# Performance work log

Hardware: AMD Instinct MI355X
Metric: run time of the kernel (lower is better)

Reference implementation:

```python
import jax, jax.numpy as jnp
import numpy as np

N_NODES = 20000
N_EDGES = 160000
N_GRAPHS = 64
IN_DIM = 1304  # 1280 + 24
NEG_SLOPE = 0.2


def gat_conv(x, src, dst, W, a_src, a_dst, b, heads, out_ch):
    """PyG-style GATConv (source_to_target flow, self loops already appended).
    x: [N, in], W: [in, heads*out], a_src/a_dst: [heads, out], b: [heads*out].
    Returns [N, heads*out] (concat=True)."""
    N = x.shape[0]
    h = (x @ W).reshape(N, heads, out_ch)                 # [N, H, C]
    e_src = jnp.sum(h * a_src[None], axis=-1)             # [N, H]
    e_dst = jnp.sum(h * a_dst[None], axis=-1)             # [N, H]
    e = jax.nn.leaky_relu(e_src[src] + e_dst[dst], NEG_SLOPE)  # [E, H]
    # softmax over incoming edges of each destination node
    e_max = jax.ops.segment_max(e, dst, num_segments=N)   # [N, H]
    e_exp = jnp.exp(e - e_max[dst])
    denom = jax.ops.segment_sum(e_exp, dst, num_segments=N)
    alpha = e_exp / (denom[dst] + 1e-16)                  # [E, H]
    msg = h[src] * alpha[:, :, None]                      # [E, H, C]
    out = jax.ops.segment_sum(msg, dst, num_segments=N)   # [N, H, C]
    return out.reshape(N, heads * out_ch) + b


def setup_inputs() -> dict:
    key = jax.random.key(0)
    ks = jax.random.split(key, 20)
    x = jax.random.normal(ks[0], (N_NODES, IN_DIM), dtype=jnp.float32)
    edge_index = jax.random.randint(ks[1], (2, N_EDGES), 0, N_NODES, dtype=jnp.int32)
    phy = jax.random.normal(ks[2], (N_GRAPHS, 188), dtype=jnp.float32)
    batch = jnp.sort(jax.random.randint(ks[3], (N_NODES,), 0, N_GRAPHS, dtype=jnp.int32))

    def glorot(k, shape):
        fan_in, fan_out = shape[0], shape[-1]
        lim = jnp.sqrt(6.0 / (fan_in + fan_out))
        return jax.random.uniform(k, shape, jnp.float32, -lim, lim)

    params = {
        # conv1: GATConv(1304, 256, heads=3)
        "W1": glorot(ks[4], (IN_DIM, 3 * 256)),
        "a_src1": glorot(ks[5], (3, 256)) * 0.1,
        "a_dst1": glorot(ks[6], (3, 256)) * 0.1,
        "b1": jnp.zeros((3 * 256,), jnp.float32),
        # conv2: GATConv(768, 256, heads=1)
        "W2": glorot(ks[7], (3 * 256, 256)),
        "a_src2": glorot(ks[8], (1, 256)) * 0.1,
        "a_dst2": glorot(ks[9], (1, 256)) * 0.1,
        "b2": jnp.zeros((256,), jnp.float32),
        # fc1
        "fc1_w1": glorot(ks[10], (188, 128)), "fc1_b1": jnp.zeros((128,), jnp.float32),
        "fc1_w2": glorot(ks[11], (128, 128)), "fc1_b2": jnp.zeros((128,), jnp.float32),
        # fc2
        "fc2_w1": glorot(ks[12], (256 + 128, 192)), "fc2_b1": jnp.zeros((192,), jnp.float32),
        "fc2_w2": glorot(ks[13], (192, 2)), "fc2_b2": jnp.zeros((2,), jnp.float32),
    }
    return {"x": x, "edge_index": edge_index, "phy": phy, "batch": batch, **params}


def reference(x, edge_index, phy, batch,
              W1, a_src1, a_dst1, b1,
              W2, a_src2, a_dst2, b2,
              fc1_w1, fc1_b1, fc1_w2, fc1_b2,
              fc2_w1, fc2_b1, fc2_w2, fc2_b2):
    N = x.shape[0]
    # add self loops (PyG GATConv default)
    loops = jnp.arange(N, dtype=edge_index.dtype)
    src = jnp.concatenate([edge_index[0], loops])
    dst = jnp.concatenate([edge_index[1], loops])

    h = gat_conv(x, src, dst, W1, a_src1, a_dst1, b1, heads=3, out_ch=256)
    h = jax.nn.relu(h)  # dropout is identity at inference
    h = gat_conv(h, src, dst, W2, a_src2, a_dst2, b2, heads=1, out_ch=256)

    # global mean pool per graph
    sums = jax.ops.segment_sum(h, batch, num_segments=N_GRAPHS)        # [B, 256]
    cnts = jax.ops.segment_sum(jnp.ones((N,), h.dtype), batch, num_segments=N_GRAPHS)
    pooled = sums / jnp.maximum(cnts, 1.0)[:, None]

    mid = jax.nn.relu(phy @ fc1_w1 + fc1_b1)
    mid = jax.nn.relu(mid @ fc1_w2 + fc1_b2)

    z = jnp.concatenate([pooled, mid], axis=1)                          # [B, 384]
    z = jax.nn.relu(z @ fc2_w1 + fc2_b1)
    logits = z @ fc2_w2 + fc2_b2
    return jax.nn.softmax(logits, axis=1)
```

## Files before the change

### kernel.cpp

```cpp
#include <hip/hip_runtime.h>
#include <hip/hip_bf16.h>
#include <math.h>

#define NN    20000
#define MP1   20224
#define NP    20096
#define E0    160000
#define EL    180000
#define NG    64
#define INDIM 1304
#define K1P   1344
#define GNT   21
#define GNX   3
#define GMB   79
#define NEG_SLOPE 0.2f
#define PCH   8

typedef __bf16 bf16x8 __attribute__((ext_vector_type(8)));
typedef __bf16 bf16x4 __attribute__((ext_vector_type(4)));
typedef float  f32x4  __attribute__((ext_vector_type(4)));

__device__ __forceinline__ void gload16(const void* g, void* l) {
    __builtin_amdgcn_global_load_lds(
        (const __attribute__((address_space(1))) void*)g,
        (__attribute__((address_space(3))) void*)l, 16, 0, 0);
}

#define BAR()  { __builtin_amdgcn_s_barrier(); asm volatile("" ::: "memory"); }
#define VMW(n) { asm volatile("s_waitcnt vmcnt(" #n ")" ::: "memory"); __builtin_amdgcn_sched_barrier(0); }

__device__ __forceinline__ void stA(const __hip_bfloat16* __restrict__ A, int bm, int kt, int mh,
                                    char* abuf, int w, int l) {
#pragma unroll
    for (int u = 0; u < 2; u++) {
        int rl = (w << 3) + (l >> 3);
        int lrow = u * 128 + mh * 64 + rl;
        int skb = ((l & 7) << 4) ^ ((rl & 7) << 4);
        const char* g = (const char*)(A + (size_t)(bm + lrow) * K1P + kt * 64) + skb;
        gload16(g, abuf + (u * 128 + mh * 64) * 128 + (w << 10));
    }
}

__device__ __forceinline__ void stB(const __hip_bfloat16* __restrict__ Bt, int bn, int kt, int nh,
                                    char* bbuf, int w, int l) {
#pragma unroll
    for (int u = 0; u < 2; u++) {
        int c = u * 2 + (w >> 2);
        int row0 = c * 64 + nh * 32;
        int rl = ((w & 3) << 3) + (l >> 3);
        int skb = ((l & 7) << 4) ^ ((rl & 7) << 4);
        const char* g = (const char*)(Bt + (size_t)(bn + row0 + rl) * K1P + kt * 64) + skb;
        gload16(g, bbuf + row0 * 128 + ((w & 3) << 10));
    }
}

__global__ __launch_bounds__(512)
void gemm256(const __hip_bfloat16* __restrict__ A,
             const __hip_bfloat16* __restrict__ Bt,
             __hip_bfloat16* __restrict__ C, int M) {
    __shared__ char lds[131072];
    const int t = threadIdx.x;
    const int w = t >> 6, l = t & 63;
    const int wm = w >> 2, wn = w & 3;
    const int fr = l & 15, fq = l >> 4;
    const int amask = (fr & 7) << 4;

    const int nwg = GMB * GNX;
    const int q8 = nwg >> 3, r8 = nwg & 7;
    const int xcd = blockIdx.x & 7, sub = blockIdx.x >> 3;
    const int logical = (xcd < r8 ? xcd * (q8 + 1) : r8 * (q8 + 1) + (xcd - r8) * q8) + sub;
    const int bm = (logical / GNX) * 256;
    const int bn = (logical % GNX) * 256;

    f32x4 acc[8][4];
#pragma unroll
    for (int i = 0; i < 8; i++)
#pragma unroll
        for (int j = 0; j < 4; j++) acc[i][j] = (f32x4){0.f, 0.f, 0.f, 0.f};

    char* A0 = lds;            char* B0 = lds + 32768;
    char* A1 = lds + 65536;    char* B1 = lds + 98304;

    stA(A, bm, 0, 0, A0, w, l);
    stB(Bt, bn, 0, 0, B0, w, l);
    stA(A, bm, 0, 1, A0, w, l);
    stB(Bt, bn, 0, 1, B0, w, l);
    stA(A, bm, 1, 0, A1, w, l);
    stB(Bt, bn, 1, 0, B1, w, l);
    VMW(8);
    BAR();

    for (int kt = 0; kt < GNT; kt++) {
        char* Ab = lds + (kt & 1) * 65536;
        char* Bb = Ab + 32768;
        char* An = lds + ((kt + 1) & 1) * 65536;
        char* Bn = An + 32768;
        bf16x8 a_c[4][2], b_c0[2][2], b_c1[2][2];

#pragma unroll
        for (int im = 0; im < 4; im++)
#pragma unroll
            for (int kk = 0; kk < 2; kk++)
                a_c[im][kk] = *(const bf16x8*)(Ab + (wm * 128 + im * 16 + fr) * 128 + ((kk * 64 + fq * 16) ^ amask));
#pragma unroll
        for (int jn = 0; jn < 2; jn++)
#pragma unroll
            for (int kk = 0; kk < 2; kk++)
                b_c0[jn][kk] = *(const bf16x8*)(Bb + (wn * 64 + jn * 16 + fr) * 128 + ((kk * 64 + fq * 16) ^ amask));
        if (kt + 1 < GNT) stA(A, bm, kt + 1, 1, An, w, l);
        BAR();
        __builtin_amdgcn_s_setprio(1);
#pragma unroll
        for (int im = 0; im < 4; im++)
#pragma unroll
            for (int jn = 0; jn < 2; jn++)
#pragma unroll
                for (int kk = 0; kk < 2; kk++)
                    acc[im][jn] = __builtin_amdgcn_mfma_f32_16x16x32_bf16(a_c[im][kk], b_c0[jn][kk], acc[im][jn], 0, 0, 0);
        __builtin_amdgcn_s_setprio(0);
        if (kt == GNT - 1) { VMW(0); } else { VMW(6); }
        BAR();

#pragma unroll
        for (int jn = 0; jn < 2; jn++)
#pragma unroll
            for (int kk = 0; kk < 2; kk++)
                b_c1[jn][kk] = *(const bf16x8*)(Bb + (wn * 64 + 32 + jn * 16 + fr) * 128 + ((kk * 64 + fq * 16) ^ amask));
        if (kt + 1 < GNT) stB(Bt, bn, kt + 1, 1, Bn, w, l);
        BAR();
        __builtin_amdgcn_s_setprio(1);
#pragma unroll
        for (int im = 0; im < 4; im++)
#pragma unroll
            for (int jn = 0; jn < 2; jn++)
#pragma unroll
                for (int kk = 0; kk < 2; kk++)
                    acc[im][2 + jn] = __builtin_amdgcn_mfma_f32_16x16x32_bf16(a_c[im][kk], b_c1[jn][kk], acc[im][2 + jn], 0, 0, 0);
        __builtin_amdgcn_s_setprio(0);
        if (kt == GNT - 1) { VMW(2); } else { VMW(10); }
        BAR();

#pragma unroll
        for (int im = 0; im < 4; im++)
#pragma unroll
            for (int kk = 0; kk < 2; kk++)
                a_c[im][kk] = *(const bf16x8*)(Ab + (wm * 128 + 64 + im * 16 + fr) * 128 + ((kk * 64 + fq * 16) ^ amask));
        if (kt + 2 < GNT) stA(A, bm, kt + 2, 0, Ab, w, l);
        BAR();
        __builtin_amdgcn_s_setprio(1);
#pragma unroll
        for (int im = 0; im < 4; im++)
#pragma unroll
            for (int jn = 0; jn < 2; jn++)
#pragma unroll
                for (int kk = 0; kk < 2; kk++)
                    acc[4 + im][jn] = __builtin_amdgcn_mfma_f32_16x16x32_bf16(a_c[im][kk], b_c0[jn][kk], acc[4 + im][jn], 0, 0, 0);
        __builtin_amdgcn_s_setprio(0);
        BAR();

        if (kt + 2 < GNT) stB(Bt, bn, kt + 2, 0, Bb, w, l);
        BAR();
        __builtin_amdgcn_s_setprio(1);
#pragma unroll
        for (int im = 0; im < 4; im++)
#pragma unroll
            for (int jn = 0; jn < 2; jn++)
#pragma unroll
                for (int kk = 0; kk < 2; kk++)
                    acc[4 + im][2 + jn] = __builtin_amdgcn_mfma_f32_16x16x32_bf16(a_c[im][kk], b_c1[jn][kk], acc[4 + im][2 + jn], 0, 0, 0);
        __builtin_amdgcn_s_setprio(0);
        if (kt + 2 < GNT) { VMW(8); }
        else if (kt + 2 == GNT) { VMW(4); }
        BAR();
    }

#pragma unroll
    for (int i = 0; i < 8; i++)
#pragma unroll
        for (int j = 0; j < 4; j++)
#pragma unroll
            for (int r = 0; r < 4; r++) {
                int row = bm + wm * 128 + i * 16 + fq * 4 + r;
                int col = bn + wn * 64 + j * 16 + fr;
                if (row < M) C[(size_t)row * 768 + col] = __float2bfloat16(acc[i][j][r]);
            }
}

template<typename CT>
__global__ __launch_bounds__(256)
void mfma_gemm(const __hip_bfloat16* __restrict__ A,
               const __hip_bfloat16* __restrict__ Bt,
               CT* __restrict__ C,
               int M, int N, int K, int NX) {
    __shared__ __hip_bfloat16 As[128 * 32];
    __shared__ __hip_bfloat16 Bs[128 * 32];
    const int t = threadIdx.x;
    const int w = t >> 6;
    const int l = t & 63;

    const int nwg = gridDim.x;
    const int q = nwg >> 3, r = nwg & 7;
    const int xcd = blockIdx.x & 7, idx = blockIdx.x >> 3;
    const int logical = (xcd < r ? xcd * (q + 1) : r * (q + 1) + (xcd - r) * q) + idx;
    const int bm = (logical / NX) * 128;
    const int bn = (logical % NX) * 128;

    const int wm = (w >> 1) * 64;
    const int wn = (w & 1) * 64;

    f32x4 acc[4][4];
#pragma unroll
    for (int i = 0; i < 4; i++)
#pragma unroll
        for (int j = 0; j < 4; j++) acc[i][j] = (f32x4){0.f, 0.f, 0.f, 0.f};

    const int sr = t >> 2;
    const int sc = (t & 3) * 8;
    const __hip_bfloat16* a0 = A  + (size_t)(bm + sr)      * K + sc;
    const __hip_bfloat16* a1 = A  + (size_t)(bm + 64 + sr) * K + sc;
    const __hip_bfloat16* b0 = Bt + (size_t)(bn + sr)      * K + sc;
    const __hip_bfloat16* b1 = Bt + (size_t)(bn + 64 + sr) * K + sc;
    char* asw0 = (char*)As + w * 1024;
    char* asw1 = (char*)As + 4096 + w * 1024;
    char* bsw0 = (char*)Bs + w * 1024;
    char* bsw1 = (char*)Bs + 4096 + w * 1024;

    const int fr = l & 15;
    const int fq = l >> 4;

    for (int k0 = 0; k0 < K; k0 += 32) {
        gload16(a0 + k0, asw0);
        gload16(a1 + k0, asw1);
        gload16(b0 + k0, bsw0);
        gload16(b1 + k0, bsw1);
        __syncthreads();
        bf16x8 av[4], bv[4];
#pragma unroll
        for (int i = 0; i < 4; i++)
            av[i] = *(const bf16x8*)&As[(wm + i * 16 + fr) * 32 + fq * 8];
#pragma unroll
        for (int j = 0; j < 4; j++)
            bv[j] = *(const bf16x8*)&Bs[(wn + j * 16 + fr) * 32 + fq * 8];
#pragma unroll
        for (int i = 0; i < 4; i++)
#pragma unroll
            for (int j = 0; j < 4; j++)
                acc[i][j] = __builtin_amdgcn_mfma_f32_16x16x32_bf16(av[i], bv[j], acc[i][j], 0, 0, 0);
        __syncthreads();
    }

#pragma unroll
    for (int i = 0; i < 4; i++) {
#pragma unroll
        for (int j = 0; j < 4; j++) {
#pragma unroll
            for (int r2 = 0; r2 < 4; r2++) {
                int row = bm + wm + i * 16 + fq * 4 + r2;
                int col = bn + wn + j * 16 + fr;
                if (row < M) {
                    if constexpr (sizeof(CT) == 2)
                        C[(size_t)row * N + col] = __float2bfloat16(acc[i][j][r2]);
                    else
                        C[(size_t)row * N + col] = acc[i][j][r2];
                }
            }
        }
    }
}

__global__ __launch_bounds__(256)
void convert_x(const float* __restrict__ X, __hip_bfloat16* __restrict__ Xb) {
    int idx = blockIdx.x * 256 + threadIdx.x;
    const int nb = K1P / 8;
    if (idx >= MP1 * nb) return;
    int row = idx / nb;
    int cb = (idx - row * nb) * 8;
    union { __hip_bfloat16 h[8]; float4 f4; } u;
    if (row < NN && cb + 8 <= INDIM) {
        const float4* p = (const float4*)(X + (size_t)row * INDIM + cb);
        float4 u0 = p[0], u1 = p[1];
        u.h[0] = __float2bfloat16(u0.x); u.h[1] = __float2bfloat16(u0.y);
        u.h[2] = __float2bfloat16(u0.z); u.h[3] = __float2bfloat16(u0.w);
        u.h[4] = __float2bfloat16(u1.x); u.h[5] = __float2bfloat16(u1.y);
        u.h[6] = __float2bfloat16(u1.z); u.h[7] = __float2bfloat16(u1.w);
    } else {
#pragma unroll
        for (int e = 0; e < 8; e++) {
            float f = (row < NN && cb + e < INDIM) ? X[(size_t)row * INDIM + cb + e] : 0.f;
            u.h[e] = __float2bfloat16(f);
        }
    }
    *(float4*)(Xb + (size_t)row * K1P + cb) = u.f4;
}

__global__ __launch_bounds__(256)
void convert_wT(const float* __restrict__ W, __hip_bfloat16* __restrict__ Wt,
                int K, int N, int Kp) {
    int idx = blockIdx.x * 256 + threadIdx.x;
    if (idx >= N * Kp) return;
    int n = idx / Kp, k = idx - n * Kp;
    float f = (k < K) ? W[(size_t)k * N + n] : 0.f;
    Wt[idx] = __float2bfloat16(f);
}

template<int H>
__global__ __launch_bounds__(256)
void compute_e(const __hip_bfloat16* __restrict__ hfeat, const float* __restrict__ a_src,
               const float* __restrict__ a_dst, float* __restrict__ esrc,
               float* __restrict__ edst, int N) {
    const int wv = threadIdx.x >> 6, lane = threadIdx.x & 63;
    const int n = blockIdx.x * 4 + wv;
    if (n >= N) return;
#pragma unroll
    for (int hd = 0; hd < H; hd++) {
        bf16x4 hv = *(const bf16x4*)(hfeat + (size_t)n * (H * 256) + hd * 256 + lane * 4);
        float ps = 0.f, pd = 0.f;
#pragma unroll
        for (int e = 0; e < 4; e++) {
            float f = (float)hv[e];
            ps += f * a_src[hd * 256 + lane * 4 + e];
            pd += f * a_dst[hd * 256 + lane * 4 + e];
        }
#pragma unroll
        for (int o = 32; o > 0; o >>= 1) {
            ps += __shfl_down(ps, o, 64);
            pd += __shfl_down(pd, o, 64);
        }
        if (lane == 0) {
            esrc[n * H + hd] = ps;
            edst[n * H + hd] = pd;
        }
    }
}

__global__ void hist_kernel(const int* __restrict__ ei, int* __restrict__ deg) {
    int e = blockIdx.x * 256 + threadIdx.x;
    if (e >= EL) return;
    int d = (e < E0) ? ei[E0 + e] : (e - E0);
    atomicAdd(&deg[d], 1);
}

__global__ __launch_bounds__(1024)
void scan_kernel(const int* __restrict__ deg, int* __restrict__ off) {
    __shared__ int wsum[16];
    __shared__ int carry_s;
    int t = threadIdx.x, lane = t & 63, wv = t >> 6;
    if (t == 0) { carry_s = 0; off[0] = 0; }
    __syncthreads();
    for (int base = 0; base < NN; base += 1024) {
        int i = base + t;
        int v = (i < NN) ? deg[i] : 0;
        int x = v;
#pragma unroll
        for (int o = 1; o < 64; o <<= 1) {
            int y = __shfl_up(x, o, 64);
            if (lane >= o) x += y;
        }
        if (lane == 63) wsum[wv] = x;
        __syncthreads();
        if (wv == 0 && lane < 16) {
            int s = wsum[lane];
#pragma unroll
            for (int o = 1; o < 16; o <<= 1) {
                int y = __shfl_up(s, o, 64);
                if (lane >= o) s += y;
            }
            wsum[lane] = s;
        }
        __syncthreads();
        int woff = (wv == 0) ? 0 : wsum[wv - 1];
        int total = wsum[15];
        if (i < NN) off[i + 1] = carry_s + woff + x;
        __syncthreads();
        if (t == 0) carry_s += total;
        __syncthreads();
    }
}

__global__ void fill_kernel(const int* __restrict__ ei, const int* __restrict__ off,
                            int* __restrict__ cur, int* __restrict__ csr) {
    int e = blockIdx.x * 256 + threadIdx.x;
    if (e >= EL) return;
    int d = (e < E0) ? ei[E0 + e] : (e - E0);
    int s = (e < E0) ? ei[e] : (e - E0);
    int pos = off[d] + atomicAdd(&cur[d], 1);
    csr[pos] = s;
}

template<int H, bool RELU, typename OutT>
__global__ __launch_bounds__(256)
void gat_aggregate(const __hip_bfloat16* __restrict__ hfeat,
                   const float* __restrict__ esrc,
                   const float* __restrict__ edst,
                   const int* __restrict__ off, const int* __restrict__ csr,
                   const float* __restrict__ bias,
                   OutT* __restrict__ out, int N) {
    const int wv = threadIdx.x >> 6, lane = threadIdx.x & 63;
    const int n = blockIdx.x * 4 + wv;
    if (n >= N) return;
    const int beg = off[n];
    const int deg = off[n + 1] - beg;

    float ed[H], m[H], den[H];
    f32x4 acc[H];
#pragma unroll
    for (int h = 0; h < H; h++) {
        ed[h] = edst[n * H + h];
        m[h] = -INFINITY;
        den[h] = 0.f;
        acc[h] = (f32x4){0.f, 0.f, 0.f, 0.f};
    }

    for (int base = 0; base < deg; base += 64) {
        const int i = base + lane;
        int s = 0;
        float lg[H];
        if (i < deg) {
            s = csr[beg + i];
#pragma unroll
            for (int h = 0; h < H; h++) {
                float v = esrc[s * H + h] + ed[h];
                lg[h] = (v >= 0.f) ? v : NEG_SLOPE * v;
            }
        } else {
#pragma unroll
            for (int h = 0; h < H; h++) lg[h] = -INFINITY;
        }
        float cm[H];
#pragma unroll
        for (int h = 0; h < H; h++) {
            cm[h] = lg[h];
#pragma unroll
            for (int o = 1; o < 64; o <<= 1)
                cm[h] = fmaxf(cm[h], __shfl_xor(cm[h], o, 64));
        }
#pragma unroll
        for (int h = 0; h < H; h++) {
            float nm = fmaxf(m[h], cm[h]);
            float sc = expf(m[h] - nm);
            den[h] *= sc;
#pragma unroll
            for (int e = 0; e < 4; e++) acc[h][e] *= sc;
            m[h] = nm;
        }
        float wgt[H];
#pragma unroll
        for (int h = 0; h < H; h++) {
            wgt[h] = (i < deg) ? expf(lg[h] - m[h]) : 0.f;
            den[h] += wgt[h];
        }
        const int cnt = min(64, deg - base);
        for (int j = 0; j < cnt; j++) {
            int sj = __shfl(s, j, 64);
#pragma unroll
            for (int h = 0; h < H; h++) {
                float wj = __shfl(wgt[h], j, 64);
                bf16x4 hv = *(const bf16x4*)(hfeat + (size_t)sj * (H * 256) + h * 256 + 4 * lane);
#pragma unroll
                for (int e = 0; e < 4; e++) acc[h][e] += wj * (float)hv[e];
            }
        }
    }
#pragma unroll
    for (int h = 0; h < H; h++) {
#pragma unroll
        for (int o = 1; o < 64; o <<= 1) den[h] += __shfl_xor(den[h], o, 64);
    }
#pragma unroll
    for (int h = 0; h < H; h++) {
        float inv = 1.f / (den[h] + 1e-16f);
        if constexpr (sizeof(OutT) == 2) {
            bf16x4 r;
#pragma unroll
            for (int e = 0; e < 4; e++) {
                float f = acc[h][e] * inv + bias[h * 256 + 4 * lane + e];
                if (RELU) f = fmaxf(f, 0.f);
                r[e] = (__bf16)f;
            }
            *(bf16x4*)((__hip_bfloat16*)out + (size_t)n * (H * 256) + h * 256 + 4 * lane) = r;
        } else {
            float4 r;
            float* rp = &r.x;
#pragma unroll
            for (int e = 0; e < 4; e++) {
                float f = acc[h][e] * inv + bias[h * 256 + 4 * lane + e];
                if (RELU) f = fmaxf(f, 0.f);
                rp[e] = f;
            }
            *(float4*)((float*)out + (size_t)n * (H * 256) + h * 256 + 4 * lane) = r;
        }
    }
}

__device__ __forceinline__ int lower_bound_batch(const int* __restrict__ batch, int key) {
    int lo = 0, hi = NN;
    while (lo < hi) {
        int mid = (lo + hi) >> 1;
        if (batch[mid] < key) lo = mid + 1; else hi = mid;
    }
    return lo;
}

__global__ __launch_bounds__(256)
void pool_partial(const float* __restrict__ out2, const int* __restrict__ batch,
                  float* __restrict__ partial, float* __restrict__ cnts) {
    const int g = blockIdx.x, c = blockIdx.y, t = threadIdx.x;
    const int s = lower_bound_batch(batch, g);
    const int e = lower_bound_batch(batch, g + 1);
    float acc = 0.f;
    for (int n = s + c; n < e; n += PCH) acc += out2[(size_t)n * 256 + t];
    partial[((size_t)g * PCH + c) * 256 + t] = acc;
    if (t == 0 && c == 0) cnts[g] = (float)(e - s);
}

__global__ __launch_bounds__(256)
void head_kernel(const float* __restrict__ phy, const float* __restrict__ partial,
                 const float* __restrict__ cnts,
                 const float* __restrict__ w11, const float* __restrict__ b11,
                 const float* __restrict__ w12, const float* __restrict__ b12,
                 const float* __restrict__ w21, const float* __restrict__ b21,
                 const float* __restrict__ w22, const float* __restrict__ b22,
                 float* __restrict__ out) {
    int g = blockIdx.x, t = threadIdx.x;
    __shared__ float ph[188];
    __shared__ float z[384];
    __shared__ float mid[128];
    __shared__ float t1[192];
    __shared__ float lg[2];
    if (t < 188) ph[t] = phy[g * 188 + t];
    {
        float s = 0.f;
#pragma unroll
        for (int c = 0; c < PCH; c++) s += partial[((size_t)g * PCH + c) * 256 + t];
        z[t] = s / fmaxf(cnts[g], 1.0f);
    }
    __syncthreads();
    if (t < 128) {
        float s = b11[t];
        for (int k = 0; k < 188; k++) s += ph[k] * w11[k * 128 + t];
        mid[t] = fmaxf(s, 0.f);
    }
    __syncthreads();
    if (t < 128) {
        float s = b12[t];
        for (int k = 0; k < 128; k++) s += mid[k] * w12[k * 128 + t];
        z[256 + t] = fmaxf(s, 0.f);
    }
    __syncthreads();
    if (t < 192) {
        float s = b21[t];
        for (int k = 0; k < 384; k++) s += z[k] * w21[k * 192 + t];
        t1[t] = fmaxf(s, 0.f);
    }
    __syncthreads();
    if (t < 2) {
        float s = b22[t];
        for (int k = 0; k < 192; k++) s += t1[k] * w22[k * 2 + t];
        lg[t] = s;
    }
    __syncthreads();
    if (t == 0) {
        float mx = fmaxf(lg[0], lg[1]);
        float e0 = expf(lg[0] - mx), e1 = expf(lg[1] - mx);
        float d = e0 + e1;
        out[g * 2 + 0] = e0 / d;
        out[g * 2 + 1] = e1 / d;
    }
}

extern "C" void kernel_launch(void* const* d_in, const int* in_sizes, int n_in,
                              void* d_out, int out_size, void* d_ws, size_t ws_size,
                              hipStream_t stream) {
    const float* x       = (const float*)d_in[0];
    const int*   ei      = (const int*)  d_in[1];
    const float* phy     = (const float*)d_in[2];
    const int*   batch   = (const int*)  d_in[3];
    const float* W1      = (const float*)d_in[4];
    const float* a_src1  = (const float*)d_in[5];
    const float* a_dst1  = (const float*)d_in[6];
    const float* b1      = (const float*)d_in[7];
    const float* W2      = (const float*)d_in[8];
    const float* a_src2  = (const float*)d_in[9];
    const float* a_dst2  = (const float*)d_in[10];
    const float* b2      = (const float*)d_in[11];
    const float* fc1_w1  = (const float*)d_in[12];
    const float* fc1_b1  = (const float*)d_in[13];
    const float* fc1_w2  = (const float*)d_in[14];
    const float* fc1_b2  = (const float*)d_in[15];
    const float* fc2_w1  = (const float*)d_in[16];
    const float* fc2_b1  = (const float*)d_in[17];
    const float* fc2_w2  = (const float*)d_in[18];
    const float* fc2_b2  = (const float*)d_in[19];
    float* out = (float*)d_out;

    char* base = (char*)d_ws;
    size_t o = 0;
    auto alloc = [&](size_t bytes) { size_t r = o; o += (bytes + 255) & ~255ULL; return r; };

    size_t o_xb   = alloc((size_t)MP1 * K1P * 2);
    size_t o_w1t  = alloc((size_t)768 * K1P * 2);
    size_t o_w2t  = alloc((size_t)256 * 768 * 2);
    size_t o_h1b  = alloc((size_t)NP * 768 * 2);
    size_t o_hob  = alloc((size_t)NP * 768 * 2);
    size_t o_es1  = alloc((size_t)NN * 3 * 4);
    size_t o_ed1  = alloc((size_t)NN * 3 * 4);
    size_t o_es2  = alloc((size_t)NN * 4);
    size_t o_ed2  = alloc((size_t)NN * 4);
    size_t o_deg  = alloc((size_t)(NN + 1) * 4);
    size_t o_off  = alloc((size_t)(NN + 1) * 4);
    size_t o_cur  = alloc((size_t)NN * 4);
    size_t o_csr  = alloc((size_t)EL * 4);
    size_t o_part = alloc((size_t)NG * PCH * 256 * 4);
    size_t o_cnts = alloc((size_t)NG * 4);

    __hip_bfloat16* xb   = (__hip_bfloat16*)(base + o_xb);
    __hip_bfloat16* w1t  = (__hip_bfloat16*)(base + o_w1t);
    __hip_bfloat16* w2t  = (__hip_bfloat16*)(base + o_w2t);
    __hip_bfloat16* h1b  = (__hip_bfloat16*)(base + o_h1b);
    __hip_bfloat16* hob  = (__hip_bfloat16*)(base + o_hob);
    __hip_bfloat16* h2b  = (__hip_bfloat16*)(base + o_xb);
    float*          out2 = (float*)(base + o_xb + (size_t)24 * 1024 * 1024);
    float* es1   = (float*)(base + o_es1);
    float* ed1   = (float*)(base + o_ed1);
    float* es2   = (float*)(base + o_es2);
    float* ed2   = (float*)(base + o_ed2);
    int*   deg   = (int*)(base + o_deg);
    int*   offs  = (int*)(base + o_off);
    int*   cur   = (int*)(base + o_cur);
    int*   csr   = (int*)(base + o_csr);
    float* part  = (float*)(base + o_part);
    float* cnts  = (float*)(base + o_cnts);

    hipMemsetAsync(deg, 0, (size_t)(NN + 1) * 4, stream);
    hipMemsetAsync(cur, 0, (size_t)NN * 4, stream);
    hipMemsetAsync(hob + (size_t)NN * 768, 0, (size_t)(NP - NN) * 768 * 2, stream);

    convert_x<<<(MP1 * (K1P / 8) + 255) / 256, 256, 0, stream>>>(x, xb);
    convert_wT<<<(768 * K1P + 255) / 256, 256, 0, stream>>>(W1, w1t, INDIM, 768, K1P);
    convert_wT<<<(256 * 768 + 255) / 256, 256, 0, stream>>>(W2, w2t, 768, 256, 768);

    hist_kernel<<<(EL + 255) / 256, 256, 0, stream>>>(ei, deg);
    scan_kernel<<<1, 1024, 0, stream>>>(deg, offs);
    fill_kernel<<<(EL + 255) / 256, 256, 0, stream>>>(ei, offs, cur, csr);

    gemm256<<<GMB * GNX, 512, 0, stream>>>(xb, w1t, h1b, NN);
    compute_e<3><<<(NN + 3) / 4, 256, 0, stream>>>(h1b, a_src1, a_dst1, es1, ed1, NN);
    gat_aggregate<3, true, __hip_bfloat16><<<(NN + 3) / 4, 256, 0, stream>>>(h1b, es1, ed1, offs, csr, b1, hob, NN);

    mfma_gemm<__hip_bfloat16><<<2 * 157, 256, 0, stream>>>(hob, w2t, h2b, NN, 256, 768, 2);
    compute_e<1><<<(NN + 3) / 4, 256, 0, stream>>>(h2b, a_src2, a_dst2, es2, ed2, NN);
    gat_aggregate<1, false, float><<<(NN + 3) / 4, 256, 0, stream>>>(h2b, es2, ed2, offs, csr, b2, out2, NN);

    pool_partial<<<dim3(NG, PCH), 256, 0, stream>>>(out2, batch, part, cnts);
    head_kernel<<<NG, 256, 0, stream>>>(phy, part, cnts,
                                        fc1_w1, fc1_b1, fc1_w2, fc1_b2,
                                        fc2_w1, fc2_b1, fc2_w2, fc2_b2, out);
}
```

Measured before the change: 280.4 us.

## Fuse attention logits into GEMM epilogue, parallelize scan, double-buffer GEMM

Computes the per-head attention logits (e_src, e_dst) inside the layer-1 GEMM epilogue from the fp32 accumulators. This removes the separate compute_e pass that re-read h1 from memory. It also replaces the single-block serial prefix scan with a three-kernel parallel scan, merges the two weight-conversion launches and the two memsets, and double-buffers LDS in the second GEMM. The costs are more launches for the scan and a small LDS reduction step in the GEMM epilogue. The double-buffered loop keeps its single trailing __syncthreads; no barrier after staging and before the LDS reads was visible in the unchanged part.

```diff
diff --git a/kernel.cpp b/kernel.cpp
--- a/kernel.cpp
+++ b/kernel.cpp
@@ -15,6 +15,7 @@
 #define GMB   79
 #define NEG_SLOPE 0.2f
 #define PCH   8
+#define NSB   20
 
 typedef __bf16 bf16x8 __attribute__((ext_vector_type(8)));
 typedef __bf16 bf16x4 __attribute__((ext_vector_type(4)));
@@ -57,7 +58,9 @@
 __global__ __launch_bounds__(512)
 void gemm256(const __hip_bfloat16* __restrict__ A,
              const __hip_bfloat16* __restrict__ Bt,
-             __hip_bfloat16* __restrict__ C, int M) {
+             __hip_bfloat16* __restrict__ C,
+             const float* __restrict__ a_src, const float* __restrict__ a_dst,
+             float* __restrict__ esrc, float* __restrict__ edst, int M) {
     __shared__ char lds[131072];
     const int t = threadIdx.x;
     const int w = t >> 6, l = t & 63;
@@ -184,6 +187,42 @@
                 int col = bn + wn * 64 + j * 16 + fr;
                 if (row < M) C[(size_t)row * 768 + col] = __float2bfloat16(acc[i][j][r]);
             }
+
+    const int head = bn >> 8;
+    float asv[4], adv[4];
+#pragma unroll
+    for (int j = 0; j < 4; j++) {
+        asv[j] = a_src[head * 256 + wn * 64 + j * 16 + fr];
+        adv[j] = a_dst[head * 256 + wn * 64 + j * 16 + fr];
+    }
+    __syncthreads();
+    float* eb = (float*)lds;
+#pragma unroll
+    for (int i = 0; i < 8; i++) {
+#pragma unroll
+        for (int r = 0; r < 4; r++) {
+            float ps = 0.f, pd = 0.f;
+#pragma unroll
+            for (int j = 0; j < 4; j++) { ps += acc[i][j][r] * asv[j]; pd += acc[i][j][r] * adv[j]; }
+#pragma unroll
+            for (int o = 8; o >= 1; o >>= 1) { ps += __shfl_xor(ps, o, 64); pd += __shfl_xor(pd, o, 64); }
+            if (fr == 0) {
+                int rowl = wm * 128 + i * 16 + fq * 4 + r;
+                eb[(rowl * 4 + wn) * 2 + 0] = ps;
+                eb[(rowl * 4 + wn) * 2 + 1] = pd;
+            }
+        }
+    }
+    __syncthreads();
+    if (t < 256) {
+        int row = bm + t;
+        if (row < M) {
+            float s = eb[t * 8 + 0] + eb[t * 8 + 2] + eb[t * 8 + 4] + eb[t * 8 + 6];
+            float d = eb[t * 8 + 1] + eb[t * 8 + 3] + eb[t * 8 + 5] + eb[t * 8 + 7];
+            esrc[row * 3 + head] = s;
+            edst[row * 3 + head] = d;
+        }
+    }
 }
 
 template<typename CT>
@@ -192,8 +231,8 @@
                const __hip_bfloat16* __restrict__ Bt,
                CT* __restrict__ C,
                int M, int N, int K, int NX) {
-    __shared__ __hip_bfloat16 As[128 * 32];
-    __shared__ __hip_bfloat16 Bs[128 * 32];
+    __shared__ __hip_bfloat16 As[2][128 * 32];
+    __shared__ __hip_bfloat16 Bs[2][128 * 32];
     const int t = threadIdx.x;
     const int w = t >> 6;
     const int l = t & 63;
@@ -220,27 +259,33 @@
     const __hip_bfloat16* a1 = A  + (size_t)(bm + 64 + sr) * K + sc;
     const __hip_bfloat16* b0 = Bt + (size_t)(bn + sr)      * K + sc;
     const __hip_bfloat16* b1 = Bt + (size_t)(bn + 64 + sr) * K + sc;
-    char* asw0 = (char*)As + w * 1024;
-    char* asw1 = (char*)As + 4096 + w * 1024;
-    char* bsw0 = (char*)Bs + w * 1024;
-    char* bsw1 = (char*)Bs + 4096 + w * 1024;
 
     const int fr = l & 15;
     const int fq = l >> 4;
-
-    for (int k0 = 0; k0 < K; k0 += 32) {
-        gload16(a0 + k0, asw0);
-        gload16(a1 + k0, asw1);
-        gload16(b0 + k0, bsw0);
-        gload16(b1 + k0, bsw1);
-        __syncthreads();
+    const int NT = K / 32;
+
+    auto stage = [&](int k0, int b) {
+        char* asb = (char*)&As[b][0];
+        char* bsb = (char*)&Bs[b][0];
+        gload16(a0 + k0, asb + w * 1024);
+        gload16(a1 + k0, asb + 4096 + w * 1024);
+        gload16(b0 + k0, bsb + w * 1024);
+        gload16(b1 + k0, bsb + 4096 + w * 1024);
+    };
+
+    stage(0, 0);
+    __syncthreads();
+
+    for (int kt = 0; kt < NT; kt++) {
+        const int cb = kt & 1;
+        if (kt + 1 < NT) stage((kt + 1) * 32, cb ^ 1);
         bf16x8 av[4], bv[4];
 #pragma unroll
         for (int i = 0; i < 4; i++)
-            av[i] = *(const bf16x8*)&As[(wm + i * 16 + fr) * 32 + fq * 8];
+            av[i] = *(const bf16x8*)&As[cb][(wm + i * 16 + fr) * 32 + fq * 8];
 #pragma unroll
         for (int j = 0; j < 4; j++)
-            bv[j] = *(const bf16x8*)&Bs[(wn + j * 16 + fr) * 32 + fq * 8];
+            bv[j] = *(const bf16x8*)&Bs[cb][(wn + j * 16 + fr) * 32 + fq * 8];
 #pragma unroll
         for (int i = 0; i < 4; i++)
 #pragma unroll
@@ -294,13 +339,21 @@
 }
 
 __global__ __launch_bounds__(256)
-void convert_wT(const float* __restrict__ W, __hip_bfloat16* __restrict__ Wt,
-                int K, int N, int Kp) {
+void convert_w_all(const float* __restrict__ W1, const float* __restrict__ W2,
+                   __hip_bfloat16* __restrict__ w1t, __hip_bfloat16* __restrict__ w2t) {
     int idx = blockIdx.x * 256 + threadIdx.x;
-    if (idx >= N * Kp) return;
-    int n = idx / Kp, k = idx - n * Kp;
-    float f = (k < K) ? W[(size_t)k * N + n] : 0.f;
-    Wt[idx] = __float2bfloat16(f);
+    const int n1 = 768 * K1P;
+    if (idx < n1) {
+        int n = idx / K1P, k = idx - n * K1P;
+        float f = (k < INDIM) ? W1[(size_t)k * 768 + n] : 0.f;
+        w1t[idx] = __float2bfloat16(f);
+    } else {
+        int i2 = idx - n1;
+        if (i2 < 256 * 768) {
+            int n = i2 / 768, k = i2 - n * 768;
+            w2t[i2] = __float2bfloat16(W2[(size_t)k * 256 + n]);
+        }
+    }
 }
 
 template<int H>
@@ -341,40 +394,52 @@
 }
 
 __global__ __launch_bounds__(1024)
-void scan_kernel(const int* __restrict__ deg, int* __restrict__ off) {
+void scan_blk(const int* __restrict__ deg, int* __restrict__ off, int* __restrict__ bsum) {
     __shared__ int wsum[16];
-    __shared__ int carry_s;
-    int t = threadIdx.x, lane = t & 63, wv = t >> 6;
-    if (t == 0) { carry_s = 0; off[0] = 0; }
-    __syncthreads();
-    for (int base = 0; base < NN; base += 1024) {
-        int i = base + t;
-        int v = (i < NN) ? deg[i] : 0;
-        int x = v;
-#pragma unroll
-        for (int o = 1; o < 64; o <<= 1) {
-            int y = __shfl_up(x, o, 64);
-            if (lane >= o) x += y;
-        }
-        if (lane == 63) wsum[wv] = x;
-        __syncthreads();
-        if (wv == 0 && lane < 16) {
-            int s = wsum[lane];
-#pragma unroll
-            for (int o = 1; o < 16; o <<= 1) {
-                int y = __shfl_up(s, o, 64);
-                if (lane >= o) s += y;
-            }
-            wsum[lane] = s;
-        }
-        __syncthreads();
-        int woff = (wv == 0) ? 0 : wsum[wv - 1];
-        int total = wsum[15];
-        if (i < NN) off[i + 1] = carry_s + woff + x;
-        __syncthreads();
-        if (t == 0) carry_s += total;
-        __syncthreads();
-    }
+    const int b = blockIdx.x, t = threadIdx.x, lane = t & 63, wv = t >> 6;
+    const int i = b * 1024 + t;
+    int v = (i < NN) ? deg[i] : 0;
+    int x = v;
+#pragma unroll
+    for (int o = 1; o < 64; o <<= 1) {
+        int y = __shfl_up(x, o, 64);
+        if (lane >= o) x += y;
+    }
+    if (lane == 63) wsum[wv] = x;
+    __syncthreads();
+    if (wv == 0 && lane < 16) {
+        int s = wsum[lane];
+#pragma unroll
+        for (int o = 1; o < 16; o <<= 1) {
+            int y = __shfl_up(s, o, 64);
+            if (lane >= o) s += y;
+        }
+        wsum[lane] = s;
+    }
+    __syncthreads();
+    int woff = (wv == 0) ? 0 : wsum[wv - 1];
+    if (i < NN) off[i + 1] = woff + x;
+    if (t == 1023) bsum[b] = wsum[15];
+}
+
+__global__ void scan_top(const int* __restrict__ bsum, int* __restrict__ boff) {
+    int lane = threadIdx.x;
+    int v = (lane < NSB) ? bsum[lane] : 0;
+    int x = v;
+#pragma unroll
+    for (int o = 1; o < 64; o <<= 1) {
+        int y = __shfl_up(x, o, 64);
+        if (lane >= o) x += y;
+    }
+    if (lane < NSB) boff[lane] = x - v;
+}
+
+__global__ __launch_bounds__(1024)
+void scan_add(int* __restrict__ off, const int* __restrict__ boff) {
+    const int b = blockIdx.x, t = threadIdx.x;
+    const int i = b * 1024 + t;
+    if (i < NN) off[i + 1] += boff[b];
+    if (b == 0 && t == 0) off[0] = 0;
 }
 
 __global__ void fill_kernel(const int* __restrict__ ei, const int* __restrict__ off,
@@ -607,9 +672,11 @@
     size_t o_es2  = alloc((size_t)NN * 4);
     size_t o_ed2  = alloc((size_t)NN * 4);
     size_t o_deg  = alloc((size_t)(NN + 1) * 4);
+    size_t o_cur  = alloc((size_t)NN * 4);
     size_t o_off  = alloc((size_t)(NN + 1) * 4);
-    size_t o_cur  = alloc((size_t)NN * 4);
     size_t o_csr  = alloc((size_t)EL * 4);
+    size_t o_bsum = alloc((size_t)NSB * 4);
+    size_t o_boff = alloc((size_t)NSB * 4);
     size_t o_part = alloc((size_t)NG * PCH * 256 * 4);
     size_t o_cnts = alloc((size_t)NG * 4);
 
@@ -625,26 +692,27 @@
     float* es2   = (float*)(base + o_es2);
     float* ed2   = (float*)(base + o_ed2);
     int*   deg   = (int*)(base + o_deg);
+    int*   cur   = (int*)(base + o_cur);
     int*   offs  = (int*)(base + o_off);
-    int*   cur   = (int*)(base + o_cur);
     int*   csr   = (int*)(base + o_csr);
+    int*   bsum  = (int*)(base + o_bsum);
+    int*   boff  = (int*)(base + o_boff);
     float* part  = (float*)(base + o_part);
     float* cnts  = (float*)(base + o_cnts);
 
-    hipMemsetAsync(deg, 0, (size_t)(NN + 1) * 4, stream);
-    hipMemsetAsync(cur, 0, (size_t)NN * 4, stream);
+    hipMemsetAsync(deg, 0, (o_cur - o_deg) + (size_t)NN * 4, stream);
     hipMemsetAsync(hob + (size_t)NN * 768, 0, (size_t)(NP - NN) * 768 * 2, stream);
 
     convert_x<<<(MP1 * (K1P / 8) + 255) / 256, 256, 0, stream>>>(x, xb);
-    convert_wT<<<(768 * K1P + 255) / 256, 256, 0, stream>>>(W1, w1t, INDIM, 768, K1P);
-    convert_wT<<<(256 * 768 + 255) / 256, 256, 0, stream>>>(W2, w2t, 768, 256, 768);
+    convert_w_all<<<(768 * K1P + 256 * 768 + 255) / 256, 256, 0, stream>>>(W1, W2, w1t, w2t);
 
     hist_kernel<<<(EL + 255) / 256, 256, 0, stream>>>(ei, deg);
-    scan_kernel<<<1, 1024, 0, stream>>>(deg, offs);
+    scan_blk<<<NSB, 1024, 0, stream>>>(deg, offs, bsum);
+    scan_top<<<1, 64, 0, stream>>>(bsum, boff);
+    scan_add<<<NSB, 1024, 0, stream>>>(offs, boff);
     fill_kernel<<<(EL + 255) / 256, 256, 0, stream>>>(ei, offs, cur, csr);
 
-    gemm256<<<GMB * GNX, 512, 0, stream>>>(xb, w1t, h1b, NN);
-    compute_e<3><<<(NN + 3) / 4, 256, 0, stream>>>(h1b, a_src1, a_dst1, es1, ed1, NN);
+    gemm256<<<GMB * GNX, 512, 0, stream>>>(xb, w1t, h1b, a_src1, a_dst1, es1, ed1, NN);
     gat_aggregate<3, true, __hip_bfloat16><<<(NN + 3) / 4, 256, 0, stream>>>(h1b, es1, ed1, offs, csr, b1, hob, NN);
 
     mfma_gemm<__hip_bfloat16><<<2 * 157, 256, 0, stream>>>(hob, w2t, h2b, NN, 256, 768, 2);
```

After: 255.0 us. -9.1%, faster.
